# Optimization experiments

Measured on AMD Instinct MI355X. Metric: run time of the kernel, lower is better.

## Reference

```python
import jax, jax.numpy as jnp
import numpy as np

B, C, H, W, D = 1, 128, 64, 64, 64
CQ = C // 8


def setup_inputs() -> dict:
    key = jax.random.key(0)
    ks = jax.random.split(key, 6)
    s = 0.05
    return {
        "x": jax.random.normal(ks[0], (B, C, H, W, D), jnp.float32),
        "y": jax.random.normal(ks[1], (B, C, H, W, D), jnp.float32),
        "Wq": jax.random.normal(ks[2], (CQ, C), jnp.float32) * s,
        "bq": jnp.zeros((CQ,), jnp.float32),
        "Wk": jax.random.normal(ks[3], (CQ, C), jnp.float32) * s,
        "bk": jnp.zeros((CQ,), jnp.float32),
        "Wv": jax.random.normal(ks[4], (C, C), jnp.float32) * s,
        "bv": jnp.zeros((C,), jnp.float32),
        # torch inits gamma to 0 (kills all attention grads); use a nonzero value
        "gamma": jax.random.normal(ks[5], (1,), jnp.float32),
    }


def _conv1x1(x, Wt, b):
    # 1x1x1 Conv3d == per-voxel linear over channels
    return jnp.einsum('bchwd,oc->bohwd', x, Wt) + b[None, :, None, None, None]


def _criss_cross(x, y, Wq, bq, Wk, bk, Wv, bv, gamma):
    Bs, Cs, Hs, Ws, Ds = x.shape
    Cq = Wq.shape[0]
    q = _conv1x1(x, Wq, bq)  # [B,Cq,H,W,D]
    k = _conv1x1(y, Wk, bk)  # [B,Cq,H,W,D]
    v = _conv1x1(x, Wv, bv)  # [B,C ,H,W,D]

    # exact transliteration of the torch permute/contiguous/view sequence
    qH = q.transpose(0, 3, 4, 1, 2).reshape(Bs * Ws * Ds, Cq, Hs).transpose(0, 2, 1)
    qW = q.transpose(0, 2, 4, 1, 3).reshape(Bs * Hs * Ds, Cq, Ws).transpose(0, 2, 1)
    qD = q.transpose(0, 2, 3, 1, 4).reshape(Bs * Hs * Ws, Cq, Ds).transpose(0, 2, 1)
    kH = k.transpose(0, 3, 4, 1, 2).reshape(Bs * Ws * Ds, Cq, Hs)
    kW = k.transpose(0, 2, 4, 1, 3).reshape(Bs * Hs * Ds, Cq, Ws)
    kD = k.transpose(0, 2, 3, 1, 4).reshape(Bs * Hs * Ws, Cq, Ds)
    vH = v.transpose(0, 3, 4, 1, 2).reshape(Bs * Ws * Ds, Cs, Hs)
    vW = v.transpose(0, 2, 4, 1, 3).reshape(Bs * Hs * Ds, Cs, Ws)
    vD = v.transpose(0, 2, 3, 1, 4).reshape(Bs * Hs * Ws, Cs, Ds)

    # INF(): -inf on the HxH diagonal, broadcast over the B*W*D batch
    inf_mask = jnp.where(jnp.eye(Hs, dtype=bool), -jnp.inf, 0.0)[None].astype(x.dtype)

    energy_H = (jnp.matmul(qH, kH) + inf_mask).reshape(Bs, Ws, Hs, Ds, Hs).transpose(0, 2, 1, 3, 4)
    energy_W = jnp.matmul(qW, kW).reshape(Bs, Hs, Ws, Ds, Ws)
    energy_D = jnp.matmul(qD, kD).reshape(Bs, Hs, Ws, Ds, Ds)

    # NOTE: original uses Softmax(dim=3) on the 5D concat -> softmax over the D axis
    concate = jax.nn.softmax(jnp.concatenate([energy_H, energy_W, energy_D], axis=4), axis=3)

    att_H = concate[..., 0:Hs].transpose(0, 2, 1, 3, 4).reshape(Bs * Ws * Ds, Hs, Hs)
    att_W = concate[..., Hs:Hs + Ws].reshape(Bs * Hs * Ds, Ws, Ws)
    att_D = concate[..., Hs + Ws:Hs + Ws + Ds].reshape(Bs * Hs * Ws, Ds, Ds)

    out_H = jnp.matmul(vH, att_H.transpose(0, 2, 1)).reshape(Bs, Ws, Cs, Hs, Ds).transpose(0, 2, 3, 1, 4)
    out_W = jnp.matmul(vW, att_W.transpose(0, 2, 1)).reshape(Bs, Hs, Cs, Ws, Ds).transpose(0, 2, 1, 3, 4)
    out_D = jnp.matmul(vD, att_D.transpose(0, 2, 1)).reshape(Bs, Hs, Cs, Ws, Ds).transpose(0, 2, 1, 3, 4)

    return gamma[0] * (out_H + out_W + out_D) + x


def reference(x, y, Wq, bq, Wk, bk, Wv, bv, gamma):
    return _criss_cross(x, y, Wq, bq, Wk, bk, Wv, bv, gamma)
```

## Files before the change

kernel.cpp:

```cpp
#include <hip/hip_runtime.h>

#define HWD 262144
#define WD  4096

typedef unsigned short bf16_t;
typedef unsigned short u16;
struct __align__(8) us4 { unsigned short x, y, z, w; };

typedef __bf16 bf16x8 __attribute__((ext_vector_type(8)));
typedef float  f32x4  __attribute__((ext_vector_type(4)));

__device__ inline float b2f(unsigned short u) {
    return __uint_as_float(((unsigned int)u) << 16);
}
__device__ inline unsigned short f2b(float f) {
    unsigned int u = __float_as_uint(f);
    u += 0x7fff + ((u >> 16) & 1);
    return (unsigned short)(u >> 16);
}

union FragU { us4 h[2]; bf16x8 v; };
__device__ inline bf16x8 ld8_a8(const u16* p) {
    FragU f; f.h[0] = *(const us4*)p; f.h[1] = *(const us4*)(p + 4); return f.v;
}
__device__ inline bf16x8 ld8_a16(const u16* p) {
    return *(const bf16x8*)p;
}

__global__ __launch_bounds__(256) void conv_v_kernel(
    const float* __restrict__ x, const float* __restrict__ Wv,
    const float* __restrict__ bv, bf16_t* __restrict__ v)
{
    __shared__ float Xs[16][64];
    __shared__ float Ws[16][132];
    const int tid = threadIdx.x;
    const int n0  = blockIdx.x * 64;
    const int og  = tid >> 4, ng = tid & 15;
    const int o0  = og * 8,  nn0 = ng * 4;
    float acc[8][4];
#pragma unroll
    for (int r = 0; r < 8; ++r) {
        const float b = bv[o0 + r];
        acc[r][0] = b; acc[r][1] = b; acc[r][2] = b; acc[r][3] = b;
    }
    for (int k0 = 0; k0 < 128; k0 += 16) {
        __syncthreads();
#pragma unroll
        for (int i = 0; i < 4; ++i) {
            const int e = tid + i * 256;
            Xs[e >> 6][e & 63] = x[(k0 + (e >> 6)) * HWD + n0 + (e & 63)];
        }
#pragma unroll
        for (int i = 0; i < 8; ++i) {
            const int e = tid + i * 256;
            Ws[e >> 7][e & 127] = Wv[(e & 127) * 128 + k0 + (e >> 7)];
        }
        __syncthreads();
#pragma unroll
        for (int kk = 0; kk < 16; ++kk) {
            const float4 xv = *(const float4*)&Xs[kk][nn0];
            const float4 wa = *(const float4*)&Ws[kk][o0];
            const float4 wb = *(const float4*)&Ws[kk][o0 + 4];
            const float w[8] = {wa.x, wa.y, wa.z, wa.w, wb.x, wb.y, wb.z, wb.w};
#pragma unroll
            for (int r = 0; r < 8; ++r) {
                acc[r][0] += w[r] * xv.x; acc[r][1] += w[r] * xv.y;
                acc[r][2] += w[r] * xv.z; acc[r][3] += w[r] * xv.w;
            }
        }
    }
#pragma unroll
    for (int r = 0; r < 8; ++r) {
        us4 o; o.x = f2b(acc[r][0]); o.y = f2b(acc[r][1]);
        o.z = f2b(acc[r][2]); o.w = f2b(acc[r][3]);
        *(us4*)&v[(size_t)(o0 + r) * HWD + n0 + nn0] = o;
    }
}

__global__ __launch_bounds__(256) void conv_qk_kernel(
    const float* __restrict__ x, const float* __restrict__ y,
    const float* __restrict__ Wq, const float* __restrict__ bq,
    const float* __restrict__ Wk, const float* __restrict__ bk,
    bf16_t* __restrict__ q, bf16_t* __restrict__ k)
{
    const float* src; const float* W; const float* b; bf16_t* dst;
    if (blockIdx.y == 0) { src = x; W = Wq; b = bq; dst = q; }
    else                 { src = y; W = Wk; b = bk; dst = k; }
    __shared__ float Ws[16][132];
    const int tid = threadIdx.x;
#pragma unroll
    for (int i = 0; i < 8; ++i) {
        const int e = tid + i * 256;
        Ws[e >> 7][e & 127] = W[e];
    }
    __syncthreads();
    const int n = blockIdx.x * 512 + tid * 2;
    float acc[16][2];
#pragma unroll
    for (int o = 0; o < 16; ++o) { acc[o][0] = b[o]; acc[o][1] = b[o]; }
    for (int c0 = 0; c0 < 128; c0 += 4) {
        float2 xv[4];
#pragma unroll
        for (int j = 0; j < 4; ++j) xv[j] = *(const float2*)&src[(c0 + j) * HWD + n];
#pragma unroll
        for (int o = 0; o < 16; ++o) {
            const float4 w = *(const float4*)&Ws[o][c0];
            acc[o][0] += w.x * xv[0].x + w.y * xv[1].x + w.z * xv[2].x + w.w * xv[3].x;
            acc[o][1] += w.x * xv[0].y + w.y * xv[1].y + w.z * xv[2].y + w.w * xv[3].y;
        }
    }
#pragma unroll
    for (int o = 0; o < 16; ++o) {
        unsigned int p = (unsigned int)f2b(acc[o][0]) |
                         ((unsigned int)f2b(acc[o][1]) << 16);
        *(unsigned int*)&dst[(size_t)o * HWD + n] = p;
    }
}

__global__ __launch_bounds__(256) void t_wd_kernel(
    const bf16_t* __restrict__ src, bf16_t* __restrict__ dst)
{
    const int h = blockIdx.x, c = blockIdx.y;
    __shared__ bf16_t tile[64][68];
    const size_t base = (size_t)c * HWD + h * WD;
    const int tid = threadIdx.x;
#pragma unroll
    for (int i = 0; i < 4; ++i) {
        const int f = (tid + i * 256) * 4;
        const int w = f >> 6, d = f & 63;
        const us4 val = *(const us4*)&src[base + w * 64 + d];
        tile[w][d] = val.x; tile[w][d + 1] = val.y;
        tile[w][d + 2] = val.z; tile[w][d + 3] = val.w;
    }
    __syncthreads();
#pragma unroll
    for (int i = 0; i < 4; ++i) {
        const int f = (tid + i * 256) * 4;
        const int d = f >> 6, w0 = f & 63;
        us4 o; o.x = tile[w0][d]; o.y = tile[w0 + 1][d];
        o.z = tile[w0 + 2][d]; o.w = tile[w0 + 3][d];
        *(us4*)&dst[base + d * 64 + w0] = o;
    }
}

__global__ __launch_bounds__(256) void t_hd_kernel(
    const bf16_t* __restrict__ src, bf16_t* __restrict__ dst)
{
    const int w = blockIdx.x, c = blockIdx.y;
    __shared__ bf16_t tile[64][68];
    const size_t cb = (size_t)c * HWD;
    const int tid = threadIdx.x;
#pragma unroll
    for (int i = 0; i < 4; ++i) {
        const int f = (tid + i * 256) * 4;
        const int h = f >> 6, d0 = f & 63;
        const us4 val = *(const us4*)&src[cb + h * WD + w * 64 + d0];
        tile[h][d0] = val.x; tile[h][d0 + 1] = val.y;
        tile[h][d0 + 2] = val.z; tile[h][d0 + 3] = val.w;
    }
    __syncthreads();
#pragma unroll
    for (int i = 0; i < 4; ++i) {
        const int f = (tid + i * 256) * 4;
        const int d = f >> 6, h0 = f & 63;
        us4 o; o.x = tile[h0][d]; o.y = tile[h0 + 1][d];
        o.z = tile[h0 + 2][d]; o.w = tile[h0 + 3][d];
        *(us4*)&dst[cb + w * WD + d * 64 + h0] = o;
    }
}

template<bool MASK>
__device__ __forceinline__ void cc_phase(
    const u16* __restrict__ qp, const u16* __restrict__ kp,
    const u16* __restrict__ vp, const size_t base, const int tid,
    u16 (*Qt)[36], u16 (*Kt)[36], u16 (*Vs)[72],
    float (*EA)[68], u16 (*PB)[72], float (*red)[64], f32x4* acc)
{
    const int w  = tid >> 6;
    const int l  = tid & 63;
    const int lg = l >> 4, lr = l & 15;

    __syncthreads();
    us4 vreg[8];
#pragma unroll
    for (int i = 0; i < 8; ++i) {
        const int f = (tid + i * 256) * 4;
        vreg[i] = *(const us4*)&vp[(size_t)(f >> 6) * HWD + base + (f & 63)];
    }
    {
        const int j = tid & 63, c0 = (tid >> 6) * 4;
        const size_t gb = base + j;
        us4 qv, kv;
        qv.x = qp[(size_t)(c0 + 0) * HWD + gb];
        qv.y = qp[(size_t)(c0 + 1) * HWD + gb];
        qv.z = qp[(size_t)(c0 + 2) * HWD + gb];
        qv.w = qp[(size_t)(c0 + 3) * HWD + gb];
        kv.x = kp[(size_t)(c0 + 0) * HWD + gb];
        kv.y = kp[(size_t)(c0 + 1) * HWD + gb];
        kv.z = kp[(size_t)(c0 + 2) * HWD + gb];
        kv.w = kp[(size_t)(c0 + 3) * HWD + gb];
        *(us4*)&Qt[j][c0] = qv;
        *(us4*)&Kt[j][c0] = kv;
    }
    __syncthreads();
    {
        const bf16x8 bk = ld8_a8(&Kt[16 * w + lr][8 * lg]);
#pragma unroll
        for (int ti = 0; ti < 4; ++ti) {
            const bf16x8 aq = ld8_a8(&Qt[16 * ti + lr][8 * lg]);
            f32x4 e = {0.f, 0.f, 0.f, 0.f};
            e = __builtin_amdgcn_mfma_f32_16x16x32_bf16(aq, bk, e, 0, 0, 0);
#pragma unroll
            for (int r = 0; r < 4; ++r)
                EA[16 * ti + 4 * lg + r][16 * w + lr] = e[r];
        }
    }
    __syncthreads();
    {
        const int j = tid & 63, seg = tid >> 6;
        float vals[16];
        float m = -1e30f;
#pragma unroll
        for (int i = 0; i < 16; ++i) {
            float vv = EA[seg * 16 + i][j];
            if (MASK && (seg * 16 + i) == j) vv = -1e30f;
            vals[i] = vv; m = fmaxf(m, vv);
        }
        red[seg][j] = m;
        __syncthreads();
        m = fmaxf(fmaxf(red[0][j], red[1][j]), fmaxf(red[2][j], red[3][j]));
        float ss = 0.f;
#pragma unroll
        for (int i = 0; i < 16; ++i) { vals[i] = __expf(vals[i] - m); ss += vals[i]; }
        __syncthreads();
        red[seg][j] = ss;
        __syncthreads();
        ss = red[0][j] + red[1][j] + red[2][j] + red[3][j];
        const float inv = 1.f / ss;
        const int odd = j & 1;
#pragma unroll
        for (int ii = 0; ii < 8; ++ii) {
            const float plo = vals[ii] * inv;
            const float phi = vals[8 + ii] * inv;
            const float olo = __shfl_xor(plo, 1);
            const float ohi = __shfl_xor(phi, 1);
            const int   i   = odd ? 8 + ii : ii;
            const float a   = odd ? ohi : plo;
            const float b   = odd ? phi : olo;
            const unsigned pk = (unsigned)f2b(a) | ((unsigned)f2b(b) << 16);
            *(unsigned*)&PB[seg * 16 + i][j & ~1] = pk;
        }
    }
#pragma unroll
    for (int i = 0; i < 8; ++i) {
        const int f = (tid + i * 256) * 4;
        *(us4*)&Vs[f >> 6][f & 63] = vreg[i];
    }
    __syncthreads();
#pragma unroll
    for (int ks = 0; ks < 2; ++ks) {
        const bf16x8 bp = ld8_a16(&PB[16 * w + lr][32 * ks + 8 * lg]);
#pragma unroll
        for (int tm = 0; tm < 8; ++tm) {
            const bf16x8 av = ld8_a16(&Vs[16 * tm + lr][32 * ks + 8 * lg]);
            acc[tm] = __builtin_amdgcn_mfma_f32_16x16x32_bf16(av, bp, acc[tm], 0, 0, 0);
        }
    }
}

__global__ __launch_bounds__(256) void cc_wd_kernel(
    const bf16_t* __restrict__ q,  const bf16_t* __restrict__ k,
    const bf16_t* __restrict__ v,
    const bf16_t* __restrict__ qT, const bf16_t* __restrict__ kT,
    const bf16_t* __restrict__ vT,
    const float* __restrict__ x, const float* __restrict__ gamma,
    float* __restrict__ out)
{
    const int s   = blockIdx.x;
    const int hh  = blockIdx.y;
    const int tid = threadIdx.x;
    __shared__ __align__(16) u16 Qt[64][36];
    __shared__ __align__(16) u16 Kt[64][36];
    __shared__ __align__(16) u16 Vs[128][72];
    __shared__ __align__(16) float EA[64][68];
    __shared__ float red[4][64];
    u16 (*PB)[72] = (u16(*)[72])EA;
    f32x4 acc[8];
#pragma unroll
    for (int i = 0; i < 8; ++i) acc[i] = (f32x4){0.f, 0.f, 0.f, 0.f};
    {
        const int rr = tid >> 2, slot = tid & 3;
        us4 z; z.x = z.y = z.z = z.w = 0;
        *(us4*)&Qt[rr][16 + 4 * slot] = z;
        *(us4*)&Kt[rr][16 + 4 * slot] = z;
    }
    const size_t base = (size_t)hh * WD + s * 64;
    for (int phase = 0; phase < 2; ++phase) {
        const u16* qp = phase ? q : qT;
        const u16* kp = phase ? k : kT;
        const u16* vp = phase ? v : vT;
        cc_phase<false>(qp, kp, vp, base, tid, Qt, Kt, Vs, EA, PB, red, acc);
    }
    const int w = tid >> 6, l = tid & 63, lg = l >> 4, lr = l & 15;
    const int dd = 16 * w + lr;
    const float g = gamma[0];
#pragma unroll
    for (int tm = 0; tm < 8; ++tm)
#pragma unroll
        for (int r = 0; r < 4; ++r) {
            const int c = 16 * tm + 4 * lg + r;
            const size_t o = (size_t)(2 * s + (c >> 6)) * HWD +
                             (size_t)hh * WD + (size_t)(c & 63) * 64 + dd;
            out[o] = g * acc[tm][r] + x[o];
        }
}

__global__ __launch_bounds__(256) void cc_h_kernel(
    const bf16_t* __restrict__ qH, const bf16_t* __restrict__ kH,
    const bf16_t* __restrict__ vH,
    const float* __restrict__ gamma, float* __restrict__ out)
{
    const int t   = blockIdx.x;
    const int ww  = blockIdx.y;
    const int tid = threadIdx.x;
    __shared__ __align__(16) u16 Qt[64][36];
    __shared__ __align__(16) u16 Kt[64][36];
    __shared__ __align__(16) u16 Vs[128][72];
    __shared__ __align__(16) float EA[64][68];
    __shared__ float red[4][64];
    u16 (*PB)[72] = (u16(*)[72])EA;
    f32x4 acc[8];
#pragma unroll
    for (int i = 0; i < 8; ++i) acc[i] = (f32x4){0.f, 0.f, 0.f, 0.f};
    {
        const int rr = tid >> 2, slot = tid & 3;
        us4 z; z.x = z.y = z.z = z.w = 0;
        *(us4*)&Qt[rr][16 + 4 * slot] = z;
        *(us4*)&Kt[rr][16 + 4 * slot] = z;
    }
    const size_t base = (size_t)ww * WD + t * 64;
    cc_phase<true>(qH, kH, vH, base, tid, Qt, Kt, Vs, EA, PB, red, acc);

    const int w = tid >> 6, l = tid & 63, lg = l >> 4, lr = l & 15;
    const int dd = 16 * w + lr;
    const float g = gamma[0];
#pragma unroll
    for (int tm = 0; tm < 8; ++tm)
#pragma unroll
        for (int r = 0; r < 4; ++r) {
            const int c = 16 * tm + 4 * lg + r;
            const size_t o = (size_t)(2 * t + (c >> 6)) * HWD +
                             (size_t)(c & 63) * WD + (size_t)ww * 64 + dd;
            out[o] += g * acc[tm][r];
        }
}

extern "C" void kernel_launch(void* const* d_in, const int* in_sizes, int n_in,
                              void* d_out, int out_size, void* d_ws, size_t ws_size,
                              hipStream_t stream)
{
    const float* x     = (const float*)d_in[0];
    const float* y     = (const float*)d_in[1];
    const float* Wq    = (const float*)d_in[2];
    const float* bq    = (const float*)d_in[3];
    const float* Wk    = (const float*)d_in[4];
    const float* bk    = (const float*)d_in[5];
    const float* Wv    = (const float*)d_in[6];
    const float* bv    = (const float*)d_in[7];
    const float* gamma = (const float*)d_in[8];
    float* out = (float*)d_out;

    bf16_t* A0 = (bf16_t*)d_ws;
    bf16_t* v  = A0;
    bf16_t* q  = A0 + (size_t)128 * HWD;
    bf16_t* k  = A0 + (size_t)144 * HWD;
    bf16_t* A1 = A0 + (size_t)160 * HWD;
    bf16_t* A2 = A1 + (size_t)160 * HWD;

    conv_v_kernel <<<4096, 256, 0, stream>>>(x, Wv, bv, v);
    conv_qk_kernel<<<dim3(512, 2), 256, 0, stream>>>(x, y, Wq, bq, Wk, bk, q, k);
    t_wd_kernel   <<<dim3(64, 160), 256, 0, stream>>>(A0, A1);
    t_hd_kernel   <<<dim3(64, 160), 256, 0, stream>>>(A0, A2);
    cc_wd_kernel  <<<dim3(64, 64), 256, 0, stream>>>(
        q, k, v, A1 + (size_t)128 * HWD, A1 + (size_t)144 * HWD, A1, x, gamma, out);
    cc_h_kernel   <<<dim3(64, 64), 256, 0, stream>>>(
        A2 + (size_t)128 * HWD, A2 + (size_t)144 * HWD, A2, gamma, out);
}
```

Before: 628.0 us.

## Move 1x1 conv projections to bf16 MFMA with split-precision hi/lo operands

Replaces the scalar FP32 FMA conv kernels for V and Q/K projections with MFMA 16x16x32 bf16 kernels. Both weights and inputs are split into bf16 high and low parts, and three MFMAs per tile (hh, hl, lh) approximate FP32 accuracy. This aims to cut the compute cost of the projection stage, in exchange for conversion work, extra LDS staging, and narrower 2-byte scattered stores.

```diff
diff --git a/kernel.cpp b/kernel.cpp
--- a/kernel.cpp
+++ b/kernel.cpp
@@ -27,93 +27,145 @@
     return *(const bf16x8*)p;
 }
 
-__global__ __launch_bounds__(256) void conv_v_kernel(
+struct HL { bf16x8 h, l; };
+__device__ inline HL split8(const float* w8) {
+    FragU H, L;
+    unsigned short hh[8], ll[8];
+#pragma unroll
+    for (int t = 0; t < 8; ++t) {
+        hh[t] = f2b(w8[t]);
+        ll[t] = f2b(w8[t] - b2f(hh[t]));
+    }
+    H.h[0].x = hh[0]; H.h[0].y = hh[1]; H.h[0].z = hh[2]; H.h[0].w = hh[3];
+    H.h[1].x = hh[4]; H.h[1].y = hh[5]; H.h[1].z = hh[6]; H.h[1].w = hh[7];
+    L.h[0].x = ll[0]; L.h[0].y = ll[1]; L.h[0].z = ll[2]; L.h[0].w = ll[3];
+    L.h[1].x = ll[4]; L.h[1].y = ll[5]; L.h[1].z = ll[6]; L.h[1].w = ll[7];
+    HL r; r.h = H.v; r.l = L.v; return r;
+}
+
+__global__ __launch_bounds__(512, 4) void conv_v_mfma(
     const float* __restrict__ x, const float* __restrict__ Wv,
     const float* __restrict__ bv, bf16_t* __restrict__ v)
 {
-    __shared__ float Xs[16][64];
-    __shared__ float Ws[16][132];
-    const int tid = threadIdx.x;
-    const int n0  = blockIdx.x * 64;
-    const int og  = tid >> 4, ng = tid & 15;
-    const int o0  = og * 8,  nn0 = ng * 4;
-    float acc[8][4];
-#pragma unroll
-    for (int r = 0; r < 8; ++r) {
-        const float b = bv[o0 + r];
-        acc[r][0] = b; acc[r][1] = b; acc[r][2] = b; acc[r][3] = b;
-    }
-    for (int k0 = 0; k0 < 128; k0 += 16) {
-        __syncthreads();
-#pragma unroll
-        for (int i = 0; i < 4; ++i) {
-            const int e = tid + i * 256;
-            Xs[e >> 6][e & 63] = x[(k0 + (e >> 6)) * HWD + n0 + (e & 63)];
-        }
-#pragma unroll
-        for (int i = 0; i < 8; ++i) {
-            const int e = tid + i * 256;
-            Ws[e >> 7][e & 127] = Wv[(e & 127) * 128 + k0 + (e >> 7)];
-        }
-        __syncthreads();
-#pragma unroll
-        for (int kk = 0; kk < 16; ++kk) {
-            const float4 xv = *(const float4*)&Xs[kk][nn0];
-            const float4 wa = *(const float4*)&Ws[kk][o0];
-            const float4 wb = *(const float4*)&Ws[kk][o0 + 4];
-            const float w[8] = {wa.x, wa.y, wa.z, wa.w, wb.x, wb.y, wb.z, wb.w};
-#pragma unroll
-            for (int r = 0; r < 8; ++r) {
-                acc[r][0] += w[r] * xv.x; acc[r][1] += w[r] * xv.y;
-                acc[r][2] += w[r] * xv.z; acc[r][3] += w[r] * xv.w;
-            }
-        }
-    }
-#pragma unroll
-    for (int r = 0; r < 8; ++r) {
-        us4 o; o.x = f2b(acc[r][0]); o.y = f2b(acc[r][1]);
-        o.z = f2b(acc[r][2]); o.w = f2b(acc[r][3]);
-        *(us4*)&v[(size_t)(o0 + r) * HWD + n0 + nn0] = o;
-    }
-}
-
-__global__ __launch_bounds__(256) void conv_qk_kernel(
+    __shared__ __align__(16) u16 Xh[64][136];
+    __shared__ __align__(16) u16 Xl[64][136];
+    const int tid  = threadIdx.x;
+    const int lane = tid & 63;
+    const int wv   = tid >> 6;
+    const int lg = lane >> 4, lr = lane & 15;
+    const int n0 = blockIdx.x * 64;
+
+    const int m0 = wv * 16;
+    bf16x8 Ah[4], Al[4];
+#pragma unroll
+    for (int ks = 0; ks < 4; ++ks) {
+        float w8[8];
+        const float* wp = &Wv[(m0 + lr) * 128 + ks * 32 + lg * 8];
+        *(float4*)&w8[0] = *(const float4*)wp;
+        *(float4*)&w8[4] = *(const float4*)(wp + 4);
+        HL hl = split8(w8);
+        Ah[ks] = hl.h; Al[ks] = hl.l;
+    }
+
+#pragma unroll
+    for (int gi = 0; gi < 2; ++gi) {
+        const int g = wv + gi * 8;
+        float v8[8];
+#pragma unroll
+        for (int s = 0; s < 8; ++s)
+            v8[s] = x[(size_t)(g * 8 + s) * HWD + n0 + lane];
+        HL hl = split8(v8);
+        *(bf16x8*)&Xh[lane][g * 8] = hl.h;
+        *(bf16x8*)&Xl[lane][g * 8] = hl.l;
+    }
+    __syncthreads();
+
+    f32x4 acc[4];
+#pragma unroll
+    for (int ns = 0; ns < 4; ++ns) acc[ns] = (f32x4){0.f, 0.f, 0.f, 0.f};
+#pragma unroll
+    for (int ks = 0; ks < 4; ++ks) {
+#pragma unroll
+        for (int ns = 0; ns < 4; ++ns) {
+            const bf16x8 Bh = ld8_a16(&Xh[ns * 16 + lr][ks * 32 + lg * 8]);
+            const bf16x8 Bl = ld8_a16(&Xl[ns * 16 + lr][ks * 32 + lg * 8]);
+            acc[ns] = __builtin_amdgcn_mfma_f32_16x16x32_bf16(Ah[ks], Bh, acc[ns], 0, 0, 0);
+            acc[ns] = __builtin_amdgcn_mfma_f32_16x16x32_bf16(Ah[ks], Bl, acc[ns], 0, 0, 0);
+            acc[ns] = __builtin_amdgcn_mfma_f32_16x16x32_bf16(Al[ks], Bh, acc[ns], 0, 0, 0);
+        }
+    }
+#pragma unroll
+    for (int ns = 0; ns < 4; ++ns)
+#pragma unroll
+        for (int r = 0; r < 4; ++r) {
+            const int m = m0 + 4 * lg + r;
+            v[(size_t)m * HWD + n0 + ns * 16 + lr] = f2b(acc[ns][r] + bv[m]);
+        }
+}
+
+__global__ __launch_bounds__(256, 4) void conv_qk_mfma(
     const float* __restrict__ x, const float* __restrict__ y,
     const float* __restrict__ Wq, const float* __restrict__ bq,
     const float* __restrict__ Wk, const float* __restrict__ bk,
     bf16_t* __restrict__ q, bf16_t* __restrict__ k)
 {
-    const float* src; const float* W; const float* b; bf16_t* dst;
-    if (blockIdx.y == 0) { src = x; W = Wq; b = bq; dst = q; }
-    else                 { src = y; W = Wk; b = bk; dst = k; }
-    __shared__ float Ws[16][132];
-    const int tid = threadIdx.x;
-#pragma unroll
-    for (int i = 0; i < 8; ++i) {
-        const int e = tid + i * 256;
-        Ws[e >> 7][e & 127] = W[e];
-    }
-    __syncthreads();
-    const int n = blockIdx.x * 512 + tid * 2;
-    float acc[16][2];
-#pragma unroll
-    for (int o = 0; o < 16; ++o) { acc[o][0] = b[o]; acc[o][1] = b[o]; }
-    for (int c0 = 0; c0 < 128; c0 += 4) {
-        float2 xv[4];
-#pragma unroll
-        for (int j = 0; j < 4; ++j) xv[j] = *(const float2*)&src[(c0 + j) * HWD + n];
-#pragma unroll
-        for (int o = 0; o < 16; ++o) {
-            const float4 w = *(const float4*)&Ws[o][c0];
-            acc[o][0] += w.x * xv[0].x + w.y * xv[1].x + w.z * xv[2].x + w.w * xv[3].x;
-            acc[o][1] += w.x * xv[0].y + w.y * xv[1].y + w.z * xv[2].y + w.w * xv[3].y;
-        }
-    }
-#pragma unroll
-    for (int o = 0; o < 16; ++o) {
-        unsigned int p = (unsigned int)f2b(acc[o][0]) |
-                         ((unsigned int)f2b(acc[o][1]) << 16);
-        *(unsigned int*)&dst[(size_t)o * HWD + n] = p;
+    __shared__ __align__(16) u16 Sh[2][32][136];
+    __shared__ __align__(16) u16 Sl[2][32][136];
+    const int tid  = threadIdx.x;
+    const int lane = tid & 63;
+    const int wv   = tid >> 6;
+    const int lg = lane >> 4, lr = lane & 15;
+    const int n0 = blockIdx.x * 32;
+
+    const float* W    = (wv < 2) ? Wq : Wk;
+    const float* bias = (wv < 2) ? bq : bk;
+    bf16_t*      dst  = (wv < 2) ? q  : k;
+    bf16x8 Ah[4], Al[4];
+#pragma unroll
+    for (int ks = 0; ks < 4; ++ks) {
+        float w8[8];
+        const float* wp = &W[lr * 128 + ks * 32 + lg * 8];
+        *(float4*)&w8[0] = *(const float4*)wp;
+        *(float4*)&w8[4] = *(const float4*)(wp + 4);
+        HL hl = split8(w8);
+        Ah[ks] = hl.h; Al[ks] = hl.l;
+    }
+
+    {
+        const int n  = tid & 31;
+        const int kb = (tid >> 5) * 16;
+#pragma unroll
+        for (int a = 0; a < 2; ++a) {
+            const float* src = a ? y : x;
+#pragma unroll
+            for (int gg = 0; gg < 2; ++gg) {
+                float v8[8];
+#pragma unroll
+                for (int s = 0; s < 8; ++s)
+                    v8[s] = src[(size_t)(kb + gg * 8 + s) * HWD + n0 + n];
+                HL hl = split8(v8);
+                *(bf16x8*)&Sh[a][n][kb + gg * 8] = hl.h;
+                *(bf16x8*)&Sl[a][n][kb + gg * 8] = hl.l;
+            }
+        }
+    }
+    __syncthreads();
+
+    const int a  = wv >> 1;
+    const int ns = wv & 1;
+    f32x4 acc = (f32x4){0.f, 0.f, 0.f, 0.f};
+#pragma unroll
+    for (int ks = 0; ks < 4; ++ks) {
+        const bf16x8 Bh = ld8_a16(&Sh[a][ns * 16 + lr][ks * 32 + lg * 8]);
+        const bf16x8 Bl = ld8_a16(&Sl[a][ns * 16 + lr][ks * 32 + lg * 8]);
+        acc = __builtin_amdgcn_mfma_f32_16x16x32_bf16(Ah[ks], Bh, acc, 0, 0, 0);
+        acc = __builtin_amdgcn_mfma_f32_16x16x32_bf16(Ah[ks], Bl, acc, 0, 0, 0);
+        acc = __builtin_amdgcn_mfma_f32_16x16x32_bf16(Al[ks], Bh, acc, 0, 0, 0);
+    }
+#pragma unroll
+    for (int r = 0; r < 4; ++r) {
+        const int m = 4 * lg + r;
+        dst[(size_t)m * HWD + n0 + ns * 16 + lr] = f2b(acc[r] + bias[m]);
     }
 }
 
@@ -377,12 +429,12 @@
     bf16_t* A1 = A0 + (size_t)160 * HWD;
     bf16_t* A2 = A1 + (size_t)160 * HWD;
 
-    conv_v_kernel <<<4096, 256, 0, stream>>>(x, Wv, bv, v);
-    conv_qk_kernel<<<dim3(512, 2), 256, 0, stream>>>(x, y, Wq, bq, Wk, bk, q, k);
-    t_wd_kernel   <<<dim3(64, 160), 256, 0, stream>>>(A0, A1);
-    t_hd_kernel   <<<dim3(64, 160), 256, 0, stream>>>(A0, A2);
-    cc_wd_kernel  <<<dim3(64, 64), 256, 0, stream>>>(
+    conv_v_mfma  <<<4096, 512, 0, stream>>>(x, Wv, bv, v);
+    conv_qk_mfma <<<8192, 256, 0, stream>>>(x, y, Wq, bq, Wk, bk, q, k);
+    t_wd_kernel  <<<dim3(64, 160), 256, 0, stream>>>(A0, A1);
+    t_hd_kernel  <<<dim3(64, 160), 256, 0, stream>>>(A0, A2);
+    cc_wd_kernel <<<dim3(64, 64), 256, 0, stream>>>(
         q, k, v, A1 + (size_t)128 * HWD, A1 + (size_t)144 * HWD, A1, x, gamma, out);
-    cc_h_kernel   <<<dim3(64, 64), 256, 0, stream>>>(
+    cc_h_kernel  <<<dim3(64, 64), 256, 0, stream>>>(
         A2 + (size_t)128 * HWD, A2 + (size_t)144 * HWD, A2, gamma, out);
 }
```

Result: faster. 574.9 us (-8.5%).
